# Kernel tuning notes

Hardware: AMD Instinct MI355X
Metric: run time of the kernel (lower is better)

The kernel has to match this reference:

```python
import jax, jax.numpy as jnp
import numpy as np

B, L, D = 2, 2048, 2048
H, HKV, HD = 16, 4, 128
GROUPS = H // HKV


def _rope_tables(key):
    # standard RoPE cos/sin tables, shape (B, L, HD)
    inv_freq = 1.0 / (10000.0 ** (jnp.arange(0, HD, 2, dtype=jnp.float32) / HD))
    pos = jnp.arange(L, dtype=jnp.float32)
    freqs = pos[:, None] * inv_freq[None, :]          # (L, HD/2)
    emb = jnp.concatenate([freqs, freqs], axis=-1)    # (L, HD)
    cos = jnp.broadcast_to(jnp.cos(emb)[None], (B, L, HD))
    sin = jnp.broadcast_to(jnp.sin(emb)[None], (B, L, HD))
    return cos, sin


def setup_inputs() -> dict:
    key = jax.random.key(0)
    ks = jax.random.split(key, 5)
    x = jax.random.normal(ks[0], (B, L, D), dtype=jnp.float32)
    cos, sin = _rope_tables(ks[1])
    s = 1.0 / np.sqrt(D)
    Wq = jax.random.normal(ks[2], (D, D), dtype=jnp.float32) * s
    bq = jnp.zeros((D,), dtype=jnp.float32)
    Wkv = jax.random.normal(ks[3], (2 * HKV * HD, D), dtype=jnp.float32) * s
    bkv = jnp.zeros((2 * HKV * HD,), dtype=jnp.float32)
    Wo = jax.random.normal(ks[4], (D, D), dtype=jnp.float32) * s
    bo = jnp.zeros((D,), dtype=jnp.float32)
    return {"x": x, "cos": cos, "sin": sin, "Wq": Wq, "bq": bq,
            "Wkv": Wkv, "bkv": bkv, "Wo": Wo, "bo": bo}


def _rotate_half(t):
    t1, t2 = jnp.split(t, 2, axis=-1)
    return jnp.concatenate([-t2, t1], axis=-1)


def reference(x, cos, sin, Wq, bq, Wkv, bkv, Wo, bo):
    b, l, d = x.shape
    # QKV projections
    q = (x @ Wq.T + bq).reshape(b, l, H, HD)
    kv = (x @ Wkv.T + bkv).reshape(b, l, 2, HKV, HD)
    k, v = kv[:, :, 0], kv[:, :, 1]
    # RoPE (unsqueeze over head dim, layout B,L,H,D)
    c = cos[:, :, None, :]
    s = sin[:, :, None, :]
    q = q * c + _rotate_half(q) * s
    k = k * c + _rotate_half(k) * s
    # GQA: expand kv heads to query heads
    k = jnp.repeat(k, GROUPS, axis=2)
    v = jnp.repeat(v, GROUPS, axis=2)
    # causal attention (flash_attn_func equivalent math)
    scores = jnp.einsum("blhd,bmhd->bhlm", q, k) / jnp.sqrt(jnp.float32(HD))
    mask = jnp.tril(jnp.ones((l, l), dtype=bool))
    scores = jnp.where(mask[None, None], scores, jnp.finfo(scores.dtype).min)
    attn = jax.nn.softmax(scores, axis=-1)
    out = jnp.einsum("bhlm,bmhd->blhd", attn, v).reshape(b, l, H * HD)
    return out @ Wo.T + bo
```

## Files before the change

### kernel.cpp

```cpp
#include <hip/hip_runtime.h>
#include <hip/hip_bf16.h>
#include <cstddef>

constexpr int B = 2, L = 2048, D = 2048;
constexpr int H = 16, HKV = 4, HD = 128;
constexpr int GROUPS = H / HKV;
constexpr int KVD = 2 * HKV * HD;
constexpr int M_ROWS = B * L;
constexpr int QKVW = D + KVD;

typedef __attribute__((ext_vector_type(8))) short short8;
typedef __attribute__((ext_vector_type(4))) short s16x4;
typedef __attribute__((ext_vector_type(4))) float f32x4;

__device__ __forceinline__ short f2bf(float f) {
    union { float f; unsigned u; } v; v.f = f;
    unsigned r = v.u + 0x7FFFu + ((v.u >> 16) & 1u);
    return (short)(r >> 16);
}

__device__ __forceinline__ float fast_exp2(float x) {
#if __has_builtin(__builtin_amdgcn_exp2f)
    return __builtin_amdgcn_exp2f(x);
#else
    return exp2f(x);
#endif
}

__device__ __forceinline__ int invp(int pos) {
    const int b16 = pos >> 4, j = pos & 15;
    return ((b16 >> 1) << 4) + j + ((b16 & 1) << 6);
}

typedef __attribute__((address_space(1))) const void cg_void;
typedef __attribute__((address_space(3))) void lds_void;
__device__ __forceinline__ void gl_lds16(const void* g, void* l) {
    __builtin_amdgcn_global_load_lds((cg_void*)g, (lds_void*)l, 16, 0, 0);
}

__global__ __launch_bounds__(256) void cast_all(
    const float* __restrict__ x, const float* __restrict__ Wq,
    const float* __restrict__ Wkv, const float* __restrict__ Wo,
    const float* __restrict__ bq, const float* __restrict__ bkv,
    short* __restrict__ xb, short* __restrict__ wqkvb, short* __restrict__ wob,
    float* __restrict__ bqkv)
{
    constexpr int n_x   = M_ROWS * D / 4;
    constexpr int n_wq  = D * D / 4;
    constexpr int n_wkv = KVD * D / 4;
    constexpr int n_wo  = D * D / 4;
    constexpr int n_w   = n_x + n_wq + n_wkv + n_wo;
    constexpr int RPW   = D / 4;
    int i = blockIdx.x * 256 + threadIdx.x;
    if (i >= n_w) {
        const int j = i - n_w;
        float4 o;
#pragma unroll
        for (int e = 0; e < 4; ++e) {
            const int idx = j * 4 + e;
            float v;
            if (idx < D)                 v = bq[((idx >> 7) << 7) + invp(idx & 127)];
            else if (idx < D + HKV * HD) v = bkv[(((idx - D) >> 7) << 7) + invp((idx - D) & 127)];
            else                         v = bkv[idx - D];
            (&o.x)[e] = v;
        }
        ((float4*)bqkv)[j] = o;
        return;
    }
    const float* src; short* dst; int isrc;
    if (i < n_x) {
        src = x; dst = xb; isrc = i;
    } else if (i < n_x + n_wq) {
        i -= n_x; src = Wq; dst = wqkvb;
        const int fi = i / RPW, col = i % RPW;
        const int head = fi >> 7, pos = fi & 127;
        isrc = ((head << 7) + invp(pos)) * RPW + col;
    } else if (i < n_x + n_wq + n_wkv) {
        i -= n_x + n_wq; src = Wkv; dst = wqkvb + (size_t)D * D;
        const int fi = i / RPW, col = i % RPW;
        if (fi < HKV * HD) {
            isrc = (((fi >> 7) << 7) + invp(fi & 127)) * RPW + col;
        } else {
            isrc = i;
        }
    } else {
        i -= n_x + n_wq + n_wkv; src = Wo; dst = wob; isrc = i;
    }
    const float4 f = ((const float4*)src)[isrc];
    s16x4 s;
    s[0] = f2bf(f.x); s[1] = f2bf(f.y); s[2] = f2bf(f.z); s[3] = f2bf(f.w);
    ((s16x4*)dst)[i] = s;
}

template<int MODE>
__global__ __launch_bounds__(512, 2) void gemm256(
    const short* __restrict__ Ag, const short* __restrict__ Wg,
    const float* __restrict__ bias, float* __restrict__ C,
    const float* __restrict__ cosp, const float* __restrict__ sinp,
    short* __restrict__ qout, short* __restrict__ kout, short* __restrict__ vtout,
    int M, int N, int K)
{
    __shared__ __align__(1024) char smem[131072];

    const int tid = threadIdx.x;
    const int w = tid >> 6, lane = tid & 63;
    const int quad = lane >> 4, n16 = lane & 15;
    const int wr = w >> 2, wc = w & 3;

    const int nbx = gridDim.x;
    const int nwg = nbx * gridDim.y;
    int wg = blockIdx.y * nbx + blockIdx.x;
    wg = (wg & 7) * (nwg >> 3) + (wg >> 3);
    const int bm = (wg / nbx) << 8;
    const int bn = (wg % nbx) << 8;

    const int nkt = K >> 6;

    const int sbo = n16 * 64 + ((quad * 16) ^ ((n16 & 8) << 2));

    const int srow = lane >> 2;
    const int scol = ((lane & 3) * 8) ^ (((lane >> 5) & 1) << 4);

    f32x4 acc[8][4];
#pragma unroll
    for (int i = 0; i < 8; ++i)
#pragma unroll
        for (int j = 0; j < 4; ++j)
#pragma unroll
            for (int r = 0; r < 4; ++r) acc[i][j][r] = 0.f;

    short8 afr[4][2], bfr[4][2];

#define STAGE_A(k0, cb, h)                                                     \
    { _Pragma("unroll") for (int j = 0; j < 2; ++j) {                          \
        const int s  = w + j * 8;                                              \
        const int u  = s >> 1;                                                 \
        const int rg = ((u >> 2) << 3) + ((h) << 2) + (u & 3);                 \
        const int gr = bm + (rg << 4) + srow;                                  \
        const int gc = (k0) + ((s & 1) << 5) + scol;                           \
        gl_lds16(Ag + (size_t)gr * K + gc,                                     \
                 smem + (cb) * 32768 + (h) * 16384 + (s << 10)); } }

#define STAGE_B(k0, cb, h)                                                     \
    { _Pragma("unroll") for (int j = 0; j < 2; ++j) {                          \
        const int s  = w + j * 8;                                              \
        const int u  = s >> 1;                                                 \
        const int rg = ((u >> 1) << 2) + ((h) << 1) + (u & 1);                 \
        const int gr = bn + (rg << 4) + srow;                                  \
        const int gc = (k0) + ((s & 1) << 5) + scol;                           \
        gl_lds16(Wg + (size_t)gr * K + gc,                                     \
                 smem + 65536 + (cb) * 32768 + (h) * 16384 + (s << 10)); } }

#define PHASE(CB, MH, RDB, STAGE_STMT, WAIT_STMT)                              \
    {                                                                          \
        if (RDB) {                                                             \
            _Pragma("unroll") for (int nj = 0; nj < 4; ++nj)                   \
            _Pragma("unroll") for (int kk = 0; kk < 2; ++kk)                   \
                bfr[nj][kk] = *(const short8*)(smem + 65536 + (CB) * 32768 +   \
                    (nj >> 1) * 16384 +                                        \
                    ((((wc * 2 + (nj & 1)) * 2) + kk) << 10) + sbo);           \
        }                                                                      \
        _Pragma("unroll") for (int mi2 = 0; mi2 < 4; ++mi2)                    \
        _Pragma("unroll") for (int kk = 0; kk < 2; ++kk)                       \
            afr[mi2][kk] = *(const short8*)(smem + (CB) * 32768 +              \
                (MH) * 16384 + ((((wr * 4 + mi2) * 2) + kk) << 10) + sbo);     \
        STAGE_STMT;                                                            \
        WAIT_STMT;                                                             \
        __builtin_amdgcn_s_barrier();                                          \
        asm volatile("s_waitcnt lgkmcnt(0)" ::: "memory");                     \
        __builtin_amdgcn_sched_barrier(0);                                     \
        __builtin_amdgcn_s_setprio(1);                                         \
        _Pragma("unroll") for (int mi2 = 0; mi2 < 4; ++mi2)                    \
        _Pragma("unroll") for (int nj = 0; nj < 4; ++nj)                       \
        _Pragma("unroll") for (int kk = 0; kk < 2; ++kk)                       \
            acc[(MH) * 4 + mi2][nj] =                                          \
                __builtin_amdgcn_mfma_f32_16x16x32_bf16(                       \
                    afr[mi2][kk], bfr[nj][kk], acc[(MH) * 4 + mi2][nj],        \
                    0, 0, 0);                                                  \
        __builtin_amdgcn_s_setprio(0);                                         \
        asm volatile("" ::: "memory");                                         \
        __builtin_amdgcn_s_barrier();                                          \
    }

#define NOP_WAIT asm volatile("" ::: "memory")

    STAGE_A(0, 0, 0);
    STAGE_B(0, 0, 0);
    STAGE_A(0, 0, 1);
    STAGE_B(0, 0, 1);
    if (nkt > 1) {
        STAGE_A(64, 1, 0);
        STAGE_B(64, 1, 0);
        asm volatile("s_waitcnt vmcnt(4)" ::: "memory");
    } else {
        asm volatile("s_waitcnt vmcnt(0)" ::: "memory");
    }
    __builtin_amdgcn_s_barrier();

    for (int t = 0; t < nkt; t += 2) {
        const int k1 = (t + 1) << 6, k2 = (t + 2) << 6, k3 = (t + 3) << 6;
        const bool g2 = (t + 2) < nkt, g3 = (t + 3) < nkt;

        PHASE(0, 0, 1, { STAGE_A(k1, 1, 1); STAGE_B(k1, 1, 1); }, NOP_WAIT);
        PHASE(0, 1, 0, { if (g2) { STAGE_A(k2, 0, 0); STAGE_B(k2, 0, 0); } },
              { if (g2) asm volatile("s_waitcnt vmcnt(4)" ::: "memory");
                else    asm volatile("s_waitcnt vmcnt(0)" ::: "memory"); });

        PHASE(1, 0, 1, { if (g2) { STAGE_A(k2, 0, 1); STAGE_B(k2, 0, 1); } }, NOP_WAIT);
        PHASE(1, 1, 0, { if (g3) { STAGE_A(k3, 1, 0); STAGE_B(k3, 1, 0); } },
              { if (g3) asm volatile("s_waitcnt vmcnt(4)" ::: "memory");
                else    asm volatile("s_waitcnt vmcnt(0)" ::: "memory"); });
    }

#undef PHASE
#undef STAGE_A
#undef STAGE_B
#undef NOP_WAIT

    if (MODE == 0) {
#pragma unroll
        for (int mh = 0; mh < 2; ++mh)
#pragma unroll
            for (int mi2 = 0; mi2 < 4; ++mi2)
#pragma unroll
                for (int r = 0; r < 4; ++r) {
                    const int row = bm + wr * 128 + mh * 64 + mi2 * 16 + quad * 4 + r;
#pragma unroll
                    for (int nh = 0; nh < 2; ++nh)
#pragma unroll
                        for (int ni2 = 0; ni2 < 2; ++ni2) {
                            const int col = bn + wc * 64 + nh * 32 + ni2 * 16 + n16;
                            C[(size_t)row * N + col] =
                                acc[mh * 4 + mi2][nh * 2 + ni2][r] + bias[col];
                        }
                }
    } else {
        short* const T = (short*)smem;
        __syncthreads();
        if (bn < D + HKV * HD) {
#pragma unroll
            for (int mh = 0; mh < 2; ++mh)
#pragma unroll
                for (int mi2 = 0; mi2 < 4; ++mi2)
#pragma unroll
                    for (int r = 0; r < 4; ++r) {
                        const int rl = wr * 128 + mh * 64 + mi2 * 16 + quad * 4 + r;
                        const int row = bm + rl;
                        const float* csrow = cosp + (size_t)row * HD;
                        const float* snrow = sinp + (size_t)row * HD;
                        const int sw = ((rl >> 2) & 7) << 4;
#pragma unroll
                        for (int nh = 0; nh < 2; ++nh) {
                            const int cl = wc * 64 + nh * 32 + n16;
                            const int iif = (wc & 1) * 32 + nh * 16 + n16;
                            const float a  = acc[mh * 4 + mi2][nh * 2 + 0][r] + bias[bn + cl];
                            const float bb = acc[mh * 4 + mi2][nh * 2 + 1][r] + bias[bn + cl + 16];
                            const float olo = a * csrow[iif]       - bb * snrow[iif];
                            const float ohi = bb * csrow[iif + 64] + a * snrow[iif + 64];
                            *(short*)((char*)T + ((rl * 512 + cl * 2) ^ sw))        = f2bf(olo);
                            *(short*)((char*)T + ((rl * 512 + (cl + 16) * 2) ^ sw)) = f2bf(ohi);
                        }
                    }
            __syncthreads();
            const bool isK = (bn >= D);
#pragma unroll
            for (int it = 0; it < 16; ++it) {
                const int idx = it * 512 + tid;
                const int rl = idx >> 5, c8 = idx & 31;
                const short8 v = *(const short8*)((char*)T +
                    ((rl * 512 + c8 * 16) ^ (((rl >> 2) & 7) << 4)));
                const int row = bm + rl;
                if (!isK) {
                    *(short8*)&qout[(size_t)row * D + bn + c8 * 8] = v;
                } else {
                    const int ck = bn - D + c8 * 8;
                    const int hk = ck >> 7, dk = ck & 127;
                    const int b_ = row >> 11, l_ = row & (L - 1);
                    *(short8*)&kout[((size_t)(b_ * HKV + hk) * L + l_) * HD + dk] = v;
                }
            }
        } else {
#pragma unroll
            for (int mh = 0; mh < 2; ++mh)
#pragma unroll
                for (int mi2 = 0; mi2 < 4; ++mi2) {
                    const int l0 = wr * 128 + mh * 64 + mi2 * 16 + quad * 4;
#pragma unroll
                    for (int nh = 0; nh < 2; ++nh)
#pragma unroll
                        for (int ni2 = 0; ni2 < 2; ++ni2) {
                            const int cl = wc * 64 + nh * 32 + ni2 * 16 + n16;
                            const float bs = bias[bn + cl];
                            s16x4 sv;
#pragma unroll
                            for (int r = 0; r < 4; ++r)
                                sv[r] = f2bf(acc[mh * 4 + mi2][nh * 2 + ni2][r] + bs);
                            *(s16x4*)((char*)T + ((cl * 512 + l0 * 2) ^ ((cl & 7) << 4))) = sv;
                        }
                }
            __syncthreads();
#pragma unroll
            for (int it = 0; it < 16; ++it) {
                const int idx = it * 512 + tid;
                const int cvr = idx >> 5, l8 = idx & 31;
                const short8 v = *(const short8*)((char*)T +
                    ((cvr * 512 + l8 * 16) ^ ((cvr & 7) << 4)));
                const int cv = bn - (D + HKV * HD) + cvr;
                const int hv = cv >> 7, dv = cv & 127;
                const int b_ = bm >> 11;
                const int lg = (bm & (L - 1)) + l8 * 8;
                *(short8*)&vtout[((size_t)(b_ * HKV + hv) * HD + dv) * L + lg] = v;
            }
        }
    }
}

__global__ __launch_bounds__(512, 2) void gemm_out(
    const short* __restrict__ Ag, const short* __restrict__ Wg,
    const float* __restrict__ bias, float* __restrict__ C,
    int M, int N, int K)
{
    __shared__ __align__(1024) char smem[98304];

    const int tid = threadIdx.x;
    const int w = tid >> 6, lane = tid & 63;
    const int quad = lane >> 4, n16 = lane & 15;
    const int wr = w >> 2, wc = w & 3;

    const int nbx = gridDim.x;
    const int nwg = nbx * gridDim.y;
    int wg = blockIdx.y * nbx + blockIdx.x;
    wg = (wg & 7) * (nwg >> 3) + (wg >> 3);
    const int bm = (wg / nbx) << 7;
    const int bn = (wg % nbx) << 8;

    const int nkt = K >> 6;

    const int sbo = n16 * 64 + ((quad * 16) ^ ((n16 & 8) << 2));
    const int srow = lane >> 2;
    const int scol = ((lane & 3) * 8) ^ (((lane >> 5) & 1) << 4);

    f32x4 acc[4][4];
#pragma unroll
    for (int i = 0; i < 4; ++i)
#pragma unroll
        for (int j = 0; j < 4; ++j)
#pragma unroll
            for (int r = 0; r < 4; ++r) acc[i][j][r] = 0.f;

    short8 afr[4], bfr[4];

#define OSTAGE_A(k0, cb, kh)                                                   \
    { const int gr = bm + (w << 4) + srow;                                     \
      const int gc = (k0) + ((kh) << 5) + scol;                                \
      gl_lds16(Ag + (size_t)gr * K + gc,                                       \
               smem + (cb) * 16384 + (kh) * 8192 + (w << 10)); }

#define OSTAGE_B(k0, cb, kh)                                                   \
    { _Pragma("unroll") for (int j = 0; j < 2; ++j) {                          \
        const int s = w + j * 8;                                               \
        const int gr = bn + (s << 4) + srow;                                   \
        const int gc = (k0) + ((kh) << 5) + scol;                              \
        gl_lds16(Wg + (size_t)gr * K + gc,                                     \
                 smem + 32768 + (cb) * 32768 + (kh) * 16384 + (s << 10)); } }

#define OPHASE(CB, KH, STAGE_STMT, WAIT_STMT)                                  \
    {                                                                          \
        _Pragma("unroll") for (int mi = 0; mi < 4; ++mi)                       \
            afr[mi] = *(const short8*)(smem + (CB) * 16384 + (KH) * 8192 +     \
                ((wr * 4 + mi) << 10) + sbo);                                  \
        _Pragma("unroll") for (int nj = 0; nj < 4; ++nj)                       \
            bfr[nj] = *(const short8*)(smem + 32768 + (CB) * 32768 +           \
                (KH) * 16384 + ((wc * 4 + nj) << 10) + sbo);                   \
        STAGE_STMT;                                                            \
        WAIT_STMT;                                                             \
        __builtin_amdgcn_s_barrier();                                          \
        asm volatile("s_waitcnt lgkmcnt(0)" ::: "memory");                     \
        __builtin_amdgcn_sched_barrier(0);                                     \
        __builtin_amdgcn_s_setprio(1);                                         \
        _Pragma("unroll") for (int mi = 0; mi < 4; ++mi)                       \
        _Pragma("unroll") for (int nj = 0; nj < 4; ++nj)                       \
            acc[mi][nj] = __builtin_amdgcn_mfma_f32_16x16x32_bf16(             \
                afr[mi], bfr[nj], acc[mi][nj], 0, 0, 0);                       \
        __builtin_amdgcn_s_setprio(0);                                         \
        asm volatile("" ::: "memory");                                         \
        __builtin_amdgcn_s_barrier();                                          \
    }

#define ONOP asm volatile("" ::: "memory")

    OSTAGE_A(0, 0, 0);
    OSTAGE_B(0, 0, 0);
    OSTAGE_A(0, 0, 1);
    OSTAGE_B(0, 0, 1);
    if (nkt > 1) {
        OSTAGE_A(64, 1, 0);
        OSTAGE_B(64, 1, 0);
        asm volatile("s_waitcnt vmcnt(3)" ::: "memory");
    } else {
        asm volatile("s_waitcnt vmcnt(0)" ::: "memory");
    }
    __builtin_amdgcn_s_barrier();

    for (int t = 0; t < nkt; t += 2) {
        const int k1 = (t + 1) << 6, k2 = (t + 2) << 6, k3 = (t + 3) << 6;
        const bool g2 = (t + 2) < nkt, g3 = (t + 3) < nkt;

        OPHASE(0, 0, { OSTAGE_A(k1, 1, 1); OSTAGE_B(k1, 1, 1); }, ONOP);
        OPHASE(0, 1, { if (g2) { OSTAGE_A(k2, 0, 0); OSTAGE_B(k2, 0, 0); } },
               { if (g2) asm volatile("s_waitcnt vmcnt(3)" ::: "memory");
                 else    asm volatile("s_waitcnt vmcnt(0)" ::: "memory"); });

        OPHASE(1, 0, { if (g2) { OSTAGE_A(k2, 0, 1); OSTAGE_B(k2, 0, 1); } }, ONOP);
        OPHASE(1, 1, { if (g3) { OSTAGE_A(k3, 1, 0); OSTAGE_B(k3, 1, 0); } },
               { if (g3) asm volatile("s_waitcnt vmcnt(3)" ::: "memory");
                 else    asm volatile("s_waitcnt vmcnt(0)" ::: "memory"); });
    }

#undef OPHASE
#undef OSTAGE_A
#undef OSTAGE_B
#undef ONOP

#pragma unroll
    for (int mi = 0; mi < 4; ++mi)
#pragma unroll
        for (int r = 0; r < 4; ++r) {
            const int row = bm + wr * 64 + mi * 16 + quad * 4 + r;
#pragma unroll
            for (int nj = 0; nj < 4; ++nj) {
                const int col = bn + wc * 64 + nj * 16 + n16;
                C[(size_t)row * N + col] = acc[mi][nj][r] + bias[col];
            }
        }
}

__global__ __launch_bounds__(512) void attn_mfma4(
    const short* __restrict__ qb_, const short* __restrict__ kb_,
    const short* __restrict__ vtb_, short* __restrict__ ob)
{
    __shared__ __align__(16) char smem[86016];
    short* const KsB  = (short*)smem;
    short* const VtB  = (short*)(smem + 32768);
    short* const PbB  = (short*)(smem + 65536);
    float* const Rbuf = (float*)smem;

    const int hkv = blockIdx.y, b = blockIdx.z;
    const int tid = threadIdx.x;
    const int w = tid >> 6, lane = tid & 63;
    const int quad = lane >> 4, n16 = lane & 15;
    const int h   = hkv * GROUPS + (w & 3);
    const int kh  = (w >> 2) * 32;
    const int khg = (w >> 2) * 4;

    const size_t kbase  = (size_t)(b * HKV + hkv) * L * HD;
    const size_t vtbase = (size_t)(b * HKV + hkv) * HD * L;
    const float c1 = 0.12751845f;
    const float c0 = -28.853901f;

    short8 ones;
#pragma unroll
    for (int i = 0; i < 8; ++i) ones[i] = (short)0x3F80;

    const int kr = lane >> 4;
    const int kg_sw = lane & 15;
    const int vr = lane >> 3;
    const int vg_sw = lane & 7;

    short* const myPb = PbB + w * (2 * 16 * 40);

#pragma unroll 1
    for (int phase = 0; phase < 2; ++phase) {
        const int qidx = phase ? (63 - (int)blockIdx.x) : (int)blockIdx.x;
        const int qb0 = qidx * 32;
        const int ntiles = (qidx >> 1) + 1;

        short8 qf[2][4];
#pragma unroll
        for (int rt = 0; rt < 2; ++rt)
#pragma unroll
            for (int kk = 0; kk < 4; ++kk)
                qf[rt][kk] = *(const short8*)&qb_[
                    ((size_t)(b * L + qb0 + rt * 16 + n16)) * D + h * HD + kk * 32 + quad * 8];

        f32x4 oacc[2][8], lacc[2];
#pragma unroll
        for (int rt = 0; rt < 2; ++rt) {
#pragma unroll
            for (int r = 0; r < 4; ++r) lacc[rt][r] = 0.f;
#pragma unroll
            for (int nt = 0; nt < 8; ++nt)
#pragma unroll
                for (int r = 0; r < 4; ++r) oacc[rt][nt][r] = 0.f;
        }

        __syncthreads();

        {
            const short* kg = kb_ + kbase;
            const short* vg = vtb_ + vtbase;
#pragma unroll
            for (int j = 0; j < 2; ++j) {
                const int chunk = w * 2 + j;
                const int r = chunk * 4 + kr;
                gl_lds16(kg + r * HD + (kg_sw ^ (r & 15)) * 8, KsB + chunk * 512);
            }
#pragma unroll
            for (int j = 0; j < 2; ++j) {
                const int chunk = w * 2 + j;
                const int d = chunk * 8 + vr;
                gl_lds16(vg + (size_t)d * L + (vg_sw ^ (d & 7)) * 8, VtB + chunk * 512);
            }
        }

        for (int kt = 0; kt < ntiles; ++kt) {
            const int buf = kt & 1;
            __syncthreads();

            if (kt + 1 < ntiles) {
                const short* kg = kb_ + kbase + (size_t)((kt + 1) * 64) * HD;
                const short* vg = vtb_ + vtbase + (kt + 1) * 64;
#pragma unroll
                for (int j = 0; j < 2; ++j) {
                    const int chunk = w * 2 + j;
                    const int r = chunk * 4 + kr;
                    gl_lds16(kg + r * HD + (kg_sw ^ (r & 15)) * 8,
                             KsB + (buf ^ 1) * 8192 + chunk * 512);
                }
#pragma unroll
                for (int j = 0; j < 2; ++j) {
                    const int chunk = w * 2 + j;
                    const int d = chunk * 8 + vr;
                    gl_lds16(vg + (size_t)d * L + (vg_sw ^ (d & 7)) * 8,
                             VtB + (buf ^ 1) * 8192 + chunk * 512);
                }
            }

            const short* Ks = KsB + buf * 8192;
            const short* Vt = VtB + buf * 8192;

            f32x4 s[2][2];
#pragma unroll
            for (int rt = 0; rt < 2; ++rt)
#pragma unroll
                for (int ktl = 0; ktl < 2; ++ktl)
#pragma unroll
                    for (int r = 0; r < 4; ++r) s[rt][ktl][r] = 0.f;
#pragma unroll
            for (int kk = 0; kk < 4; ++kk) {
                short8 kf[2];
#pragma unroll
                for (int ktl = 0; ktl < 2; ++ktl) {
                    const int row = kh + ktl * 16 + n16;
                    kf[ktl] = *(const short8*)&Ks[row * 128 + ((kk * 4 + quad) ^ n16) * 8];
                }
#pragma unroll
                for (int rt = 0; rt < 2; ++rt)
#pragma unroll
                    for (int ktl = 0; ktl < 2; ++ktl)
                        s[rt][ktl] = __builtin_amdgcn_mfma_f32_16x16x32_bf16(
                            qf[rt][kk], kf[ktl], s[rt][ktl], 0, 0, 0);
            }

            const bool lastt = (kt == ntiles - 1);
#pragma unroll
            for (int rt = 0; rt < 2; ++rt) {
#pragma unroll
                for (int ktl = 0; ktl < 2; ++ktl) {
                    const int key0 = kt * 64 + kh + ktl * 16 + n16;
#pragma unroll
                    for (int r = 0; r < 4; ++r) {
                        float sv = s[rt][ktl][r];
                        if (lastt) {
                            const int qi = qb0 + rt * 16 + quad * 4 + r;
                            sv = (key0 <= qi) ? sv : -1e30f;
                        }
                        const float e = fast_exp2(sv * c1 + c0);
                        myPb[(rt * 16 + quad * 4 + r) * 40 + ktl * 16 + n16] = f2bf(e);
                    }
                }
            }
            asm volatile("s_waitcnt lgkmcnt(0)" ::: "memory");

            short8 pf[2];
#pragma unroll
            for (int rt = 0; rt < 2; ++rt)
                pf[rt] = *(const short8*)&myPb[(rt * 16 + n16) * 40 + quad * 8];
#pragma unroll
            for (int rt = 0; rt < 2; ++rt)
                lacc[rt] = __builtin_amdgcn_mfma_f32_16x16x32_bf16(pf[rt], ones, lacc[rt], 0, 0, 0);
#pragma unroll
            for (int nt = 0; nt < 8; ++nt) {
                const short8 vf = *(const short8*)&Vt[
                    (nt * 16 + n16) * 64 + ((khg + quad) ^ (n16 & 7)) * 8];
#pragma unroll
                for (int rt = 0; rt < 2; ++rt)
                    oacc[rt][nt] = __builtin_amdgcn_mfma_f32_16x16x32_bf16(pf[rt], vf, oacc[rt][nt], 0, 0, 0);
            }
        }

        __syncthreads();
        if (w >= 4) {
            float* rp = Rbuf + ((size_t)(w - 4) * 64 + lane) * 76;
#pragma unroll
            for (int rt = 0; rt < 2; ++rt)
#pragma unroll
                for (int nt = 0; nt < 8; ++nt)
                    *(f32x4*)&rp[(rt * 8 + nt) * 4] = oacc[rt][nt];
            *(f32x4*)&rp[64] = lacc[0];
            *(f32x4*)&rp[68] = lacc[1];
        }
        __syncthreads();
        if (w < 4) {
            const float* rp = Rbuf + ((size_t)w * 64 + lane) * 76;
#pragma unroll
            for (int rt = 0; rt < 2; ++rt) {
                const f32x4 lr = *(const f32x4*)&rp[64 + rt * 4];
#pragma unroll
                for (int r = 0; r < 4; ++r) lacc[rt][r] += lr[r];
#pragma unroll
                for (int nt = 0; nt < 8; ++nt) {
                    const f32x4 o2 = *(const f32x4*)&rp[(rt * 8 + nt) * 4];
#pragma unroll
                    for (int r = 0; r < 4; ++r) oacc[rt][nt][r] += o2[r];
                }
            }
#pragma unroll
            for (int rt = 0; rt < 2; ++rt) {
#pragma unroll
                for (int r = 0; r < 4; ++r) {
                    const float inv = 1.0f / lacc[rt][r];
                    short* op = ob + ((size_t)(b * L + qb0 + rt * 16 + quad * 4 + r)) * D + h * HD + n16;
#pragma unroll
                    for (int nt = 0; nt < 8; ++nt) op[nt * 16] = f2bf(oacc[rt][nt][r] * inv);
                }
            }
        }
    }
}

extern "C" void kernel_launch(void* const* d_in, const int* in_sizes, int n_in,
                              void* d_out, int out_size, void* d_ws, size_t ws_size,
                              hipStream_t stream)
{
    const float* x    = (const float*)d_in[0];
    const float* cosp = (const float*)d_in[1];
    const float* sinp = (const float*)d_in[2];
    const float* Wq   = (const float*)d_in[3];
    const float* bq   = (const float*)d_in[4];
    const float* Wkv  = (const float*)d_in[5];
    const float* bkv  = (const float*)d_in[6];
    const float* Wo   = (const float*)d_in[7];
    const float* bo   = (const float*)d_in[8];
    float* out = (float*)d_out;

    char* p = (char*)d_ws;
    short* x_bf    = (short*)p; p += (size_t)M_ROWS * D * 2;
    short* wqkv_bf = (short*)p; p += (size_t)QKVW * D * 2;
    short* wo_bf   = (short*)p; p += (size_t)D * D * 2;
    float* b_qkv   = (float*)p; p += (size_t)QKVW * 4;
    short* q_bf    = (short*)p; p += (size_t)M_ROWS * D * 2;
    short* k_bf    = (short*)p; p += (size_t)M_ROWS * HKV * HD * 2;
    short* vt_bf   = (short*)p;
    short* attn_bf = x_bf;

    dim3 blk(256);

    cast_all<<<dim3(18435), blk, 0, stream>>>(
        x, Wq, Wkv, Wo, bq, bkv, x_bf, wqkv_bf, wo_bf, b_qkv);

    gemm256<1><<<dim3(QKVW / 256, M_ROWS / 256), dim3(512), 0, stream>>>(
        x_bf, wqkv_bf, b_qkv, nullptr, cosp, sinp, q_bf, k_bf, vt_bf,
        M_ROWS, QKVW, D);

    attn_mfma4<<<dim3(32, HKV, B), dim3(512), 0, stream>>>(q_bf, k_bf, vt_bf, attn_bf);

    gemm_out<<<dim3(D / 256, M_ROWS / 128), dim3(512), 0, stream>>>(
        attn_bf, wo_bf, bo, out, M_ROWS, D, D);
}
```

Baseline: 281.7 us.

## Double-buffer LDS fragment reads to overlap with MFMA in both GEMM kernels

Rewrites the main loops of the QKV and output-projection GEMMs so that register fragments are double-buffered. The next phase's LDS reads are issued before the current phase's MFMAs, and partial lgkmcnt waits replace the full wait. The goal is to hide LDS read latency behind matrix math and cut the stall at each phase boundary. The cost is extra VGPRs for the second fragment set and subtler hand-placed waits and barriers, where a wrong count could cause races.

```diff
diff --git a/kernel.cpp b/kernel.cpp
--- a/kernel.cpp
+++ b/kernel.cpp
@@ -37,6 +37,11 @@
 __device__ __forceinline__ void gl_lds16(const void* g, void* l) {
     __builtin_amdgcn_global_load_lds((cg_void*)g, (lds_void*)l, 16, 0, 0);
 }
+
+#define SBAR  __builtin_amdgcn_sched_barrier(0)
+#define KBAR  __builtin_amdgcn_s_barrier()
+#define LGKM(N) asm volatile("s_waitcnt lgkmcnt(" #N ")" ::: "memory")
+#define VMC(N)  asm volatile("s_waitcnt vmcnt(" #N ")" ::: "memory")
 
 __global__ __launch_bounds__(256) void cast_all(
     const float* __restrict__ x, const float* __restrict__ Wq,
@@ -129,7 +134,7 @@
 #pragma unroll
             for (int r = 0; r < 4; ++r) acc[i][j][r] = 0.f;
 
-    short8 afr[4][2], bfr[4][2];
+    short8 a0[4][2], a1[4][2], bfr[4][2];
 
 #define STAGE_A(k0, cb, h)                                                     \
     { _Pragma("unroll") for (int j = 0; j < 2; ++j) {                          \
@@ -151,71 +156,71 @@
         gl_lds16(Wg + (size_t)gr * K + gc,                                     \
                  smem + 65536 + (cb) * 32768 + (h) * 16384 + (s << 10)); } }
 
-#define PHASE(CB, MH, RDB, STAGE_STMT, WAIT_STMT)                              \
-    {                                                                          \
-        if (RDB) {                                                             \
-            _Pragma("unroll") for (int nj = 0; nj < 4; ++nj)                   \
-            _Pragma("unroll") for (int kk = 0; kk < 2; ++kk)                   \
-                bfr[nj][kk] = *(const short8*)(smem + 65536 + (CB) * 32768 +   \
-                    (nj >> 1) * 16384 +                                        \
-                    ((((wc * 2 + (nj & 1)) * 2) + kk) << 10) + sbo);           \
-        }                                                                      \
-        _Pragma("unroll") for (int mi2 = 0; mi2 < 4; ++mi2)                    \
-        _Pragma("unroll") for (int kk = 0; kk < 2; ++kk)                       \
-            afr[mi2][kk] = *(const short8*)(smem + (CB) * 32768 +              \
-                (MH) * 16384 + ((((wr * 4 + mi2) * 2) + kk) << 10) + sbo);     \
-        STAGE_STMT;                                                            \
-        WAIT_STMT;                                                             \
-        __builtin_amdgcn_s_barrier();                                          \
-        asm volatile("s_waitcnt lgkmcnt(0)" ::: "memory");                     \
-        __builtin_amdgcn_sched_barrier(0);                                     \
-        __builtin_amdgcn_s_setprio(1);                                         \
-        _Pragma("unroll") for (int mi2 = 0; mi2 < 4; ++mi2)                    \
-        _Pragma("unroll") for (int nj = 0; nj < 4; ++nj)                       \
-        _Pragma("unroll") for (int kk = 0; kk < 2; ++kk)                       \
-            acc[(MH) * 4 + mi2][nj] =                                          \
-                __builtin_amdgcn_mfma_f32_16x16x32_bf16(                       \
-                    afr[mi2][kk], bfr[nj][kk], acc[(MH) * 4 + mi2][nj],        \
-                    0, 0, 0);                                                  \
-        __builtin_amdgcn_s_setprio(0);                                         \
-        asm volatile("" ::: "memory");                                         \
-        __builtin_amdgcn_s_barrier();                                          \
-    }
-
-#define NOP_WAIT asm volatile("" ::: "memory")
-
-    STAGE_A(0, 0, 0);
-    STAGE_B(0, 0, 0);
-    STAGE_A(0, 0, 1);
-    STAGE_B(0, 0, 1);
-    if (nkt > 1) {
-        STAGE_A(64, 1, 0);
-        STAGE_B(64, 1, 0);
-        asm volatile("s_waitcnt vmcnt(4)" ::: "memory");
-    } else {
-        asm volatile("s_waitcnt vmcnt(0)" ::: "memory");
-    }
-    __builtin_amdgcn_s_barrier();
+#define RD_B(CB)                                                               \
+    { _Pragma("unroll") for (int nj = 0; nj < 4; ++nj)                         \
+      _Pragma("unroll") for (int kk = 0; kk < 2; ++kk)                         \
+        bfr[nj][kk] = *(const short8*)(smem + 65536 + (CB) * 32768 +           \
+            (nj >> 1) * 16384 + ((((wc * 2 + (nj & 1)) * 2) + kk) << 10) + sbo); }
+
+#define RD_A(DST, CB, MH)                                                      \
+    { _Pragma("unroll") for (int mi = 0; mi < 4; ++mi)                         \
+      _Pragma("unroll") for (int kk = 0; kk < 2; ++kk)                         \
+        DST[mi][kk] = *(const short8*)(smem + (CB) * 32768 + (MH) * 16384 +    \
+            ((((wr * 4 + mi) * 2) + kk) << 10) + sbo); }
+
+#define MFMA32(MH, AR)                                                         \
+    { __builtin_amdgcn_s_setprio(1);                                           \
+      _Pragma("unroll") for (int mi = 0; mi < 4; ++mi)                         \
+      _Pragma("unroll") for (int nj = 0; nj < 4; ++nj)                         \
+      _Pragma("unroll") for (int kk = 0; kk < 2; ++kk)                         \
+        acc[(MH) * 4 + mi][nj] = __builtin_amdgcn_mfma_f32_16x16x32_bf16(      \
+            AR[mi][kk], bfr[nj][kk], acc[(MH) * 4 + mi][nj], 0, 0, 0);         \
+      __builtin_amdgcn_s_setprio(0); }
+
+    STAGE_A(0, 0, 0); STAGE_B(0, 0, 0);
+    STAGE_A(0, 0, 1); STAGE_B(0, 0, 1);
+    if (nkt > 1) { STAGE_A(64, 1, 0); STAGE_B(64, 1, 0); VMC(4); }
+    else         { VMC(0); }
+    KBAR; SBAR;
+    RD_A(a0, 0, 0);
 
     for (int t = 0; t < nkt; t += 2) {
         const int k1 = (t + 1) << 6, k2 = (t + 2) << 6, k3 = (t + 3) << 6;
         const bool g2 = (t + 2) < nkt, g3 = (t + 3) < nkt;
 
-        PHASE(0, 0, 1, { STAGE_A(k1, 1, 1); STAGE_B(k1, 1, 1); }, NOP_WAIT);
-        PHASE(0, 1, 0, { if (g2) { STAGE_A(k2, 0, 0); STAGE_B(k2, 0, 0); } },
-              { if (g2) asm volatile("s_waitcnt vmcnt(4)" ::: "memory");
-                else    asm volatile("s_waitcnt vmcnt(0)" ::: "memory"); });
-
-        PHASE(1, 0, 1, { if (g2) { STAGE_A(k2, 0, 1); STAGE_B(k2, 0, 1); } }, NOP_WAIT);
-        PHASE(1, 1, 0, { if (g3) { STAGE_A(k3, 1, 0); STAGE_B(k3, 1, 0); } },
-              { if (g3) asm volatile("s_waitcnt vmcnt(4)" ::: "memory");
-                else    asm volatile("s_waitcnt vmcnt(0)" ::: "memory"); });
+        RD_B(0); SBAR;
+        RD_A(a1, 0, 1);
+        STAGE_A(k1, 1, 1); STAGE_B(k1, 1, 1);
+        LGKM(8); SBAR;
+        MFMA32(0, a0);
+        KBAR;
+        if (g2) { STAGE_A(k2, 0, 0); STAGE_B(k2, 0, 0); VMC(4); }
+        else    { VMC(0); }
+        KBAR; SBAR;
+        RD_A(a0, 1, 0);
+        LGKM(8); SBAR;
+        MFMA32(1, a1);
+        KBAR;
+        RD_B(1); SBAR;
+        RD_A(a1, 1, 1);
+        if (g2) { STAGE_A(k2, 0, 1); STAGE_B(k2, 0, 1); }
+        LGKM(8); SBAR;
+        MFMA32(0, a0);
+        KBAR;
+        if (g3) { STAGE_A(k3, 1, 0); STAGE_B(k3, 1, 0); VMC(4); }
+        else    { VMC(0); }
+        KBAR; SBAR;
+        if (g2) { RD_A(a0, 0, 0); LGKM(8); } else { LGKM(0); }
+        SBAR;
+        MFMA32(1, a1);
+        KBAR;
     }
 
-#undef PHASE
+#undef MFMA32
+#undef RD_A
+#undef RD_B
 #undef STAGE_A
 #undef STAGE_B
-#undef NOP_WAIT
 
     if (MODE == 0) {
 #pragma unroll
@@ -348,7 +353,7 @@
 #pragma unroll
             for (int r = 0; r < 4; ++r) acc[i][j][r] = 0.f;
 
-    short8 afr[4], bfr[4];
+    short8 oa0[4], ob0[4], oa1[4], ob1[4];
 
 #define OSTAGE_A(k0, cb, kh)                                                   \
     { const int gr = bm + (w << 4) + srow;                                     \
@@ -364,63 +369,63 @@
         gl_lds16(Wg + (size_t)gr * K + gc,                                     \
                  smem + 32768 + (cb) * 32768 + (kh) * 16384 + (s << 10)); } }
 
-#define OPHASE(CB, KH, STAGE_STMT, WAIT_STMT)                                  \
-    {                                                                          \
-        _Pragma("unroll") for (int mi = 0; mi < 4; ++mi)                       \
-            afr[mi] = *(const short8*)(smem + (CB) * 16384 + (KH) * 8192 +     \
-                ((wr * 4 + mi) << 10) + sbo);                                  \
-        _Pragma("unroll") for (int nj = 0; nj < 4; ++nj)                       \
-            bfr[nj] = *(const short8*)(smem + 32768 + (CB) * 32768 +           \
-                (KH) * 16384 + ((wc * 4 + nj) << 10) + sbo);                   \
-        STAGE_STMT;                                                            \
-        WAIT_STMT;                                                             \
-        __builtin_amdgcn_s_barrier();                                          \
-        asm volatile("s_waitcnt lgkmcnt(0)" ::: "memory");                     \
-        __builtin_amdgcn_sched_barrier(0);                                     \
-        __builtin_amdgcn_s_setprio(1);                                         \
-        _Pragma("unroll") for (int mi = 0; mi < 4; ++mi)                       \
-        _Pragma("unroll") for (int nj = 0; nj < 4; ++nj)                       \
-            acc[mi][nj] = __builtin_amdgcn_mfma_f32_16x16x32_bf16(             \
-                afr[mi], bfr[nj], acc[mi][nj], 0, 0, 0);                       \
-        __builtin_amdgcn_s_setprio(0);                                         \
-        asm volatile("" ::: "memory");                                         \
-        __builtin_amdgcn_s_barrier();                                          \
-    }
-
-#define ONOP asm volatile("" ::: "memory")
-
-    OSTAGE_A(0, 0, 0);
-    OSTAGE_B(0, 0, 0);
-    OSTAGE_A(0, 0, 1);
-    OSTAGE_B(0, 0, 1);
-    if (nkt > 1) {
-        OSTAGE_A(64, 1, 0);
-        OSTAGE_B(64, 1, 0);
-        asm volatile("s_waitcnt vmcnt(3)" ::: "memory");
-    } else {
-        asm volatile("s_waitcnt vmcnt(0)" ::: "memory");
-    }
-    __builtin_amdgcn_s_barrier();
+#define ORD(AD, BD, CB, KH)                                                    \
+    { _Pragma("unroll") for (int mi = 0; mi < 4; ++mi)                         \
+        AD[mi] = *(const short8*)(smem + (CB) * 16384 + (KH) * 8192 +          \
+            ((wr * 4 + mi) << 10) + sbo);                                      \
+      _Pragma("unroll") for (int nj = 0; nj < 4; ++nj)                         \
+        BD[nj] = *(const short8*)(smem + 32768 + (CB) * 32768 +                \
+            (KH) * 16384 + ((wc * 4 + nj) << 10) + sbo); }
+
+#define OMFMA(AD, BD)                                                          \
+    { __builtin_amdgcn_s_setprio(1);                                           \
+      _Pragma("unroll") for (int mi = 0; mi < 4; ++mi)                         \
+      _Pragma("unroll") for (int nj = 0; nj < 4; ++nj)                         \
+        acc[mi][nj] = __builtin_amdgcn_mfma_f32_16x16x32_bf16(                 \
+            AD[mi], BD[nj], acc[mi][nj], 0, 0, 0);                             \
+      __builtin_amdgcn_s_setprio(0); }
+
+    OSTAGE_A(0, 0, 0); OSTAGE_B(0, 0, 0);
+    OSTAGE_A(0, 0, 1); OSTAGE_B(0, 0, 1);
+    if (nkt > 1) { OSTAGE_A(64, 1, 0); OSTAGE_B(64, 1, 0); VMC(3); }
+    else         { VMC(0); }
+    KBAR; SBAR;
+    ORD(oa0, ob0, 0, 0);
 
     for (int t = 0; t < nkt; t += 2) {
         const int k1 = (t + 1) << 6, k2 = (t + 2) << 6, k3 = (t + 3) << 6;
         const bool g2 = (t + 2) < nkt, g3 = (t + 3) < nkt;
 
-        OPHASE(0, 0, { OSTAGE_A(k1, 1, 1); OSTAGE_B(k1, 1, 1); }, ONOP);
-        OPHASE(0, 1, { if (g2) { OSTAGE_A(k2, 0, 0); OSTAGE_B(k2, 0, 0); } },
-               { if (g2) asm volatile("s_waitcnt vmcnt(3)" ::: "memory");
-                 else    asm volatile("s_waitcnt vmcnt(0)" ::: "memory"); });
-
-        OPHASE(1, 0, { if (g2) { OSTAGE_A(k2, 0, 1); OSTAGE_B(k2, 0, 1); } }, ONOP);
-        OPHASE(1, 1, { if (g3) { OSTAGE_A(k3, 1, 0); OSTAGE_B(k3, 1, 0); } },
-               { if (g3) asm volatile("s_waitcnt vmcnt(3)" ::: "memory");
-                 else    asm volatile("s_waitcnt vmcnt(0)" ::: "memory"); });
+        ORD(oa1, ob1, 0, 1);
+        OSTAGE_A(k1, 1, 1); OSTAGE_B(k1, 1, 1);
+        LGKM(8); SBAR;
+        OMFMA(oa0, ob0);
+        KBAR;
+        if (g2) { OSTAGE_A(k2, 0, 0); OSTAGE_B(k2, 0, 0); VMC(3); }
+        else    { VMC(0); }
+        KBAR; SBAR;
+        ORD(oa0, ob0, 1, 0);
+        LGKM(8); SBAR;
+        OMFMA(oa1, ob1);
+        KBAR;
+        ORD(oa1, ob1, 1, 1);
+        if (g2) { OSTAGE_A(k2, 0, 1); OSTAGE_B(k2, 0, 1); }
+        LGKM(8); SBAR;
+        OMFMA(oa0, ob0);
+        KBAR;
+        if (g3) { OSTAGE_A(k3, 1, 0); OSTAGE_B(k3, 1, 0); VMC(3); }
+        else    { VMC(0); }
+        KBAR; SBAR;
+        if (g2) { ORD(oa0, ob0, 0, 0); LGKM(8); } else { LGKM(0); }
+        SBAR;
+        OMFMA(oa1, ob1);
+        KBAR;
     }
 
-#undef OPHASE
+#undef OMFMA
+#undef ORD
 #undef OSTAGE_A
 #undef OSTAGE_B
-#undef ONOP
 
 #pragma unroll
     for (int mi = 0; mi < 4; ++mi)
```

Result: slower. 298.0 us (+5.8%).
